# Kernel optimization log

Hardware: AMD Instinct MI355X
Metric: run time of the kernel (lower is better)

The kernel has to match this reference:

```python
import jax, jax.numpy as jnp
import numpy as np

DIM = 256
NUM_HEADS = 8
HEAD_DIM = DIM // NUM_HEADS
SCALE = HEAD_DIM ** -0.5
KSIZE = 5


def setup_inputs() -> dict:
    key = jax.random.key(0)
    ks = jax.random.split(key, 6)
    B, C, H, W = 8, DIM, 32, 32
    x = jax.random.normal(ks[0], (B, C, H, W), dtype=jnp.float32)
    qkv_w = jax.random.normal(ks[1], (3 * C, C), dtype=jnp.float32) * 0.02  # 1x1 conv, no bias
    proj_w = jax.random.normal(ks[2], (C, C), dtype=jnp.float32) * 0.02    # 1x1 conv
    proj_b = jax.random.normal(ks[3], (C,), dtype=jnp.float32) * 0.02
    lepe_w = jax.random.normal(ks[4], (C, 1, KSIZE, KSIZE), dtype=jnp.float32) * 0.02  # depthwise
    lepe_b = jax.random.normal(ks[5], (C,), dtype=jnp.float32) * 0.02
    return {"x": x, "qkv_w": qkv_w, "proj_w": proj_w, "proj_b": proj_b,
            "lepe_w": lepe_w, "lepe_b": lepe_b}


def _forward(x, qkv_w, proj_w, proj_b, lepe_w, lepe_b):
    B, C, H, W = x.shape
    N = H * W
    # 1x1 conv qkv: [B,3C,H,W]
    qkv = jnp.einsum('bchw,oc->bohw', x, qkv_w)
    q, k, v = jnp.split(qkv, 3, axis=1)
    # reshape to [B, heads, head_dim, N]
    qh = q.reshape(B, NUM_HEADS, HEAD_DIM, N)
    kh = k.reshape(B, NUM_HEADS, HEAD_DIM, N)
    vh = v.reshape(B, NUM_HEADS, HEAD_DIM, N)
    # attn = (q^T k) * scale, softmax over keys -> [B, heads, N, N]
    attn = jnp.einsum('bhdn,bhdm->bhnm', qh, kh)
    attn = jax.nn.softmax(attn * SCALE, axis=-1)
    # out = attn @ v^T -> [B, heads, N, head_dim] -> [B, C, H, W]
    out = jnp.einsum('bhnm,bhdm->bhdn', attn, vh).reshape(B, C, H, W)
    # LePE: depthwise conv on v (image layout) + residual add
    lepe = jax.lax.conv_general_dilated(
        v, lepe_w, window_strides=(1, 1),
        padding=[(KSIZE // 2, KSIZE // 2)] * 2,
        dimension_numbers=('NCHW', 'OIHW', 'NCHW'),
        feature_group_count=C) + lepe_b[None, :, None, None]
    out = out + lepe
    # 1x1 proj
    out = jnp.einsum('bchw,oc->bohw', out, proj_w) + proj_b[None, :, None, None]
    return out


def reference(x, qkv_w, proj_w, proj_b, lepe_w, lepe_b):
    return _forward(x, qkv_w, proj_w, proj_b, lepe_w, lepe_b)
```

## Files before the change

### kernel.cpp

```cpp
#include <hip/hip_runtime.h>

#define NB 8
#define NC 256
#define NN 1024

typedef unsigned short u16;
typedef unsigned int u32;
typedef __attribute__((ext_vector_type(8))) short short8;
typedef __attribute__((ext_vector_type(4))) float f32x4;

__device__ __forceinline__ u16 f2b(float f){ union{float ff;u32 i;}v; v.ff=f; u32 r=v.i+0x7FFFu+((v.i>>16)&1u); return (u16)(r>>16); }
__device__ __forceinline__ float b2f(u16 p){ union{u32 i;float f;}v; v.i=((u32)p)<<16; return v.f; }
__device__ __forceinline__ float pklo(u32 p){ union{u32 i;float f;}v; v.i=p<<16; return v.f; }
__device__ __forceinline__ float pkhi(u32 p){ union{u32 i;float f;}v; v.i=p&0xFFFF0000u; return v.f; }

#define QSC 0.25503486f

union FR { uint4 u; short8 s; };

__global__ void __launch_bounds__(256) k_cast(const float* __restrict__ x,
                                              u16* __restrict__ xt){
  const int n0 = blockIdx.x*64, c0 = blockIdx.y*128, b = blockIdx.z;
  const int tid = threadIdx.x;
  __shared__ u16 lt[64][136];
  #pragma unroll
  for (int cc = 0; cc < 4; cc++){
    const int c = c0 + cc*32 + (tid>>3);
    const int ns = (tid&7)*8;
    const float* src = x + ((size_t)(b*NC + c))*NN + n0 + ns;
    float4 a = *(const float4*)src;
    float4 d = *(const float4*)(src+4);
    const int cl = c - c0;
    lt[ns+0][cl] = f2b(a.x); lt[ns+1][cl] = f2b(a.y);
    lt[ns+2][cl] = f2b(a.z); lt[ns+3][cl] = f2b(a.w);
    lt[ns+4][cl] = f2b(d.x); lt[ns+5][cl] = f2b(d.y);
    lt[ns+6][cl] = f2b(d.z); lt[ns+7][cl] = f2b(d.w);
  }
  __syncthreads();
  #pragma unroll
  for (int p = 0; p < 4; p++){
    const int flat = p*256 + tid;
    const int row = flat >> 4, seg = flat & 15;
    uint4 d = *(uint4*)&lt[row][seg*8];
    *(uint4*)(xt + ((size_t)(b*NN + n0 + row))*NC + c0 + seg*8) = d;
  }
}

__global__ void __launch_bounds__(256) k_qkv(const float* __restrict__ wq,
                                             const u16* __restrict__ xt,
                                             u16* __restrict__ qt,
                                             u16* __restrict__ kt,
                                             u16* __restrict__ v){
  const int ot = blockIdx.x >> 6, rest = blockIdx.x & 63;
  const int nt = rest >> 3, b = rest & 7;
  const int o0 = ot*64;
  const int tid = threadIdx.x, wv = tid>>6, lane = tid&63;
  const int l15 = lane&15, quad = lane>>4;
  const int n0w = nt*128 + wv*32;
  __shared__ u16 swq[64][264];
  __shared__ u16 s2[4][32][72];
  #pragma unroll
  for (int i = 0; i < 16; i++){
    const int flat = i*256 + tid;
    const int row = flat >> 6, c4 = flat & 63;
    float4 a = *(const float4*)(wq + (size_t)(o0+row)*NC + c4*4);
    uint2 p;
    p.x = (u32)f2b(a.x) | ((u32)f2b(a.y)<<16);
    p.y = (u32)f2b(a.z) | ((u32)f2b(a.w)<<16);
    *(uint2*)&swq[row][c4*4] = p;
  }
  __syncthreads();
  f32x4 acc[4][2];
  #pragma unroll
  for (int mt = 0; mt < 4; mt++)
    #pragma unroll
    for (int n2 = 0; n2 < 2; n2++) acc[mt][n2] = (f32x4){0.f,0.f,0.f,0.f};
  const u16* xb = xt + ((size_t)(b*NN + n0w))*NC;
  for (int k0 = 0; k0 < 256; k0 += 32){
    FR af[4], bf[2];
    #pragma unroll
    for (int mt = 0; mt < 4; mt++)
      af[mt].u = *(uint4*)&swq[mt*16 + l15][k0 + quad*8];
    #pragma unroll
    for (int n2 = 0; n2 < 2; n2++)
      bf[n2].u = *(const uint4*)(xb + (size_t)(n2*16+l15)*NC + k0 + quad*8);
    #pragma unroll
    for (int mt = 0; mt < 4; mt++)
      #pragma unroll
      for (int n2 = 0; n2 < 2; n2++)
        acc[mt][n2] = __builtin_amdgcn_mfma_f32_16x16x32_bf16(af[mt].s, bf[n2].s, acc[mt][n2], 0,0,0);
  }
  if (ot < 8){
    const float sc = (ot < 4) ? QSC : 1.0f;
    u16* dstbase = (ot < 4) ? qt : kt;
    const int h0 = (ot < 4) ? (o0 >> 5) : ((o0-256) >> 5);
    #pragma unroll
    for (int mt = 0; mt < 4; mt++)
      #pragma unroll
      for (int n2 = 0; n2 < 2; n2++){
        uint2 w;
        w.x = (u32)f2b(acc[mt][n2][0]*sc) | ((u32)f2b(acc[mt][n2][1]*sc)<<16);
        w.y = (u32)f2b(acc[mt][n2][2]*sc) | ((u32)f2b(acc[mt][n2][3]*sc)<<16);
        *(uint2*)&s2[wv][n2*16+l15][mt*16+quad*4] = w;
      }
    __syncthreads();
    #pragma unroll
    for (int p = 0; p < 4; p++){
      const int u = p*64 + lane;
      const int hh = u >> 7, rem = u & 127;
      const int n_loc = rem >> 2, seg = rem & 3;
      uint4 d = *(uint4*)&s2[wv][n_loc][hh*32 + seg*8];
      u16* db = dstbase + ((size_t)(b*8 + h0 + hh)*NN + n0w + n_loc)*32 + seg*8;
      *(uint4*)db = d;
    }
  } else {
    const int c0 = o0 - 512;
    #pragma unroll
    for (int mt = 0; mt < 4; mt++)
      #pragma unroll
      for (int n2 = 0; n2 < 2; n2++)
        #pragma unroll
        for (int r = 0; r < 4; r++)
          v[(size_t)(b*NC + c0 + mt*16 + quad*4 + r)*NN + n0w + n2*16 + l15] = f2b(acc[mt][n2][r]);
  }
}

__global__ void __launch_bounds__(256, 4) k_attn(const u16* __restrict__ qt,
                                                 const u16* __restrict__ kt,
                                                 const u16* __restrict__ v,
                                                 const float* __restrict__ lw,
                                                 const float* __restrict__ lb,
                                                 u16* __restrict__ tt){
  const int qt2 = blockIdx.x >> 6, bh = blockIdx.x & 63;
  const int b = bh >> 3, h = bh & 7;
  const int tid = threadIdx.x;
  const int wv = tid >> 6, lane = tid & 63;
  const int l15 = lane & 15, quad = lane >> 4;
  const int qg = wv & 1, kh = wv >> 1;
  const int q0 = qt2*64 + qg*32;

  __shared__ u16 pb[4][2][16][40];
  __shared__ u16 vstage[6][32][38];
  __shared__ u16 s_out[2][32][36];
  __shared__ float mnum[2][32][33];
  __shared__ float mden[2][32];

  {
    const int rr = tid >> 5, lc2 = tid & 31;
    if (rr < 6){
      const int yy = qt2*2 - 2 + rr;
      u32* dst32 = (u32*)&vstage[rr][lc2][0];
      if (yy < 0 || yy > 31){
        #pragma unroll
        for (int j = 0; j < 19; j++) dst32[j] = 0;
      } else {
        const u16* src = v + ((size_t)(b*NC + h*32 + lc2))*NN + yy*32;
        uint4 a = *(const uint4*)src;
        uint4 b4 = *(const uint4*)(src+8);
        uint4 c4 = *(const uint4*)(src+16);
        uint4 d4 = *(const uint4*)(src+24);
        dst32[0] = 0;
        dst32[1]=a.x;  dst32[2]=a.y;  dst32[3]=a.z;  dst32[4]=a.w;
        dst32[5]=b4.x; dst32[6]=b4.y; dst32[7]=b4.z; dst32[8]=b4.w;
        dst32[9]=c4.x; dst32[10]=c4.y; dst32[11]=c4.z; dst32[12]=c4.w;
        dst32[13]=d4.x; dst32[14]=d4.y; dst32[15]=d4.z; dst32[16]=d4.w;
        dst32[17]=0; dst32[18]=0;
      }
    }
  }
  __syncthreads();

  const u16* qtb = qt + (size_t)bh*NN*32;
  const u16* ktb = kt + (size_t)bh*NN*32;
  const u16* vbp = v + (size_t)(b*256 + h*32)*NN;

  FR qa, qb_;
  qa.u  = *(const uint4*)(qtb + (size_t)(q0      + l15)*32 + quad*8);
  qb_.u = *(const uint4*)(qtb + (size_t)(q0 + 16 + l15)*32 + quad*8);

  f32x4 z = {0.f,0.f,0.f,0.f};
  f32x4 oA0 = z, oA1 = z, oB0 = z, oB1 = z;
  float denA[4] = {0.f,0.f,0.f,0.f}, denB[4] = {0.f,0.f,0.f,0.f};

  u16* pA = &pb[wv][0][0][0];
  u16* pB = &pb[wv][1][0][0];

  for (int it = 0; it < 16; it++){
    const int m0 = kh*512 + it*32;
    FR kf0, kf1, vf0, vf1;
    kf0.u = *(const uint4*)(ktb + (size_t)(m0      + l15)*32 + quad*8);
    kf1.u = *(const uint4*)(ktb + (size_t)(m0 + 16 + l15)*32 + quad*8);
    vf0.u = *(const uint4*)(vbp + (size_t)(l15     )*NN + m0 + quad*8);
    vf1.u = *(const uint4*)(vbp + (size_t)(16 + l15)*NN + m0 + quad*8);

    f32x4 sA0 = __builtin_amdgcn_mfma_f32_16x16x32_bf16(qa.s,  kf0.s, z, 0,0,0);
    f32x4 sA1 = __builtin_amdgcn_mfma_f32_16x16x32_bf16(qa.s,  kf1.s, z, 0,0,0);
    f32x4 sB0 = __builtin_amdgcn_mfma_f32_16x16x32_bf16(qb_.s, kf0.s, z, 0,0,0);
    f32x4 sB1 = __builtin_amdgcn_mfma_f32_16x16x32_bf16(qb_.s, kf1.s, z, 0,0,0);

    #pragma unroll
    for (int r = 0; r < 4; r++){
      float pA0 = __builtin_amdgcn_exp2f(sA0[r]);
      float pA1 = __builtin_amdgcn_exp2f(sA1[r]);
      float pB0 = __builtin_amdgcn_exp2f(sB0[r]);
      float pB1 = __builtin_amdgcn_exp2f(sB1[r]);
      denA[r] += pA0 + pA1;
      denB[r] += pB0 + pB1;
      const int row = (quad*4 + r)*40;
      pA[row + l15]      = (u16)(__float_as_uint(pA0)>>16);
      pA[row + 16 + l15] = (u16)(__float_as_uint(pA1)>>16);
      pB[row + l15]      = (u16)(__float_as_uint(pB0)>>16);
      pB[row + 16 + l15] = (u16)(__float_as_uint(pB1)>>16);
    }
    FR pfA, pfB;
    pfA.u = *(const uint4*)(pA + l15*40 + quad*8);
    pfB.u = *(const uint4*)(pB + l15*40 + quad*8);

    oA0 = __builtin_amdgcn_mfma_f32_16x16x32_bf16(pfA.s, vf0.s, oA0, 0,0,0);
    oA1 = __builtin_amdgcn_mfma_f32_16x16x32_bf16(pfA.s, vf1.s, oA1, 0,0,0);
    oB0 = __builtin_amdgcn_mfma_f32_16x16x32_bf16(pfB.s, vf0.s, oB0, 0,0,0);
    oB1 = __builtin_amdgcn_mfma_f32_16x16x32_bf16(pfB.s, vf1.s, oB1, 0,0,0);
  }
  #pragma unroll
  for (int r = 0; r < 4; r++){
    #pragma unroll
    for (int m = 1; m < 16; m <<= 1){
      denA[r] += __shfl_xor(denA[r], m);
      denB[r] += __shfl_xor(denB[r], m);
    }
  }
  __syncthreads();
  if (kh == 1){
    #pragma unroll
    for (int r = 0; r < 4; r++){
      mnum[qg][quad*4 + r][l15]          = oA0[r];
      mnum[qg][quad*4 + r][16 + l15]     = oA1[r];
      mnum[qg][16 + quad*4 + r][l15]     = oB0[r];
      mnum[qg][16 + quad*4 + r][16 + l15]= oB1[r];
    }
    if (l15 == 0){
      #pragma unroll
      for (int r = 0; r < 4; r++){
        mden[qg][quad*4 + r]      = denA[r];
        mden[qg][16 + quad*4 + r] = denB[r];
      }
    }
  }
  __syncthreads();
  if (kh == 0){
    u16* so = &s_out[qg][0][0];
    #pragma unroll
    for (int r = 0; r < 4; r++){
      const int q = quad*4 + r;
      const float dA = denA[r] + mden[qg][q];
      const float dB = denB[r] + mden[qg][16 + q];
      const float iA = 1.f/dA, iB = 1.f/dB;
      so[q*36 + l15]           = f2b((oA0[r] + mnum[qg][q][l15])*iA);
      so[q*36 + 16 + l15]      = f2b((oA1[r] + mnum[qg][q][16+l15])*iA);
      so[(q+16)*36 + l15]      = f2b((oB0[r] + mnum[qg][16+q][l15])*iB);
      so[(q+16)*36 + 16 + l15] = f2b((oB1[r] + mnum[qg][16+q][16+l15])*iB);
    }
    const int lc = lane & 31, qh = lane >> 5;
    float lep[16];
    const float lbias = lb[h*32 + lc];
    #pragma unroll
    for (int i = 0; i < 16; i++) lep[i] = lbias;
    const float* lwc = lw + (size_t)(h*32 + lc)*25;
    #pragma unroll
    for (int ky = 0; ky < 5; ky++){
      const u32* vr = (const u32*)&vstage[qg + ky][lc][0];
      float vv[20];
      #pragma unroll
      for (int jj = 0; jj < 10; jj++){
        u32 pk = vr[qh*8 + jj];
        vv[2*jj]   = pklo(pk);
        vv[2*jj+1] = pkhi(pk);
      }
      const float w0 = lwc[ky*5+0], w1 = lwc[ky*5+1], w2 = lwc[ky*5+2],
                  w3 = lwc[ky*5+3], w4 = lwc[ky*5+4];
      #pragma unroll
      for (int i = 0; i < 16; i++)
        lep[i] += w0*vv[i] + w1*vv[i+1] + w2*vv[i+2] + w3*vv[i+3] + w4*vv[i+4];
    }
    u16* tb = tt + ((size_t)(b*NN + q0))*NC + h*32;
    #pragma unroll
    for (int i = 0; i < 16; i++){
      const int q = qh*16 + i;
      tb[(size_t)q*NC + lc] = f2b(b2f(so[q*36 + lc]) + lep[i]);
    }
  }
}

__global__ void __launch_bounds__(256) k_proj(const float* __restrict__ wp,
                                              const u16* __restrict__ tt,
                                              const float* __restrict__ pbias,
                                              float* __restrict__ out){
  const int ot = blockIdx.x >> 6, rest = blockIdx.x & 63;
  const int nt = rest >> 3, b = rest & 7;
  const int o0 = ot*32;
  const int tid = threadIdx.x, wv = tid>>6, lane = tid&63;
  const int l15 = lane&15, quad = lane>>4;
  const int n0w = nt*128 + wv*32;
  __shared__ u16 swp[32][264];
  #pragma unroll
  for (int i = 0; i < 8; i++){
    const int flat = i*256 + tid;
    const int row = flat >> 6, c4 = flat & 63;
    float4 a = *(const float4*)(wp + (size_t)(o0+row)*NC + c4*4);
    uint2 p;
    p.x = (u32)f2b(a.x) | ((u32)f2b(a.y)<<16);
    p.y = (u32)f2b(a.z) | ((u32)f2b(a.w)<<16);
    *(uint2*)&swp[row][c4*4] = p;
  }
  __syncthreads();
  f32x4 acc[2][2];
  #pragma unroll
  for (int mt = 0; mt < 2; mt++)
    #pragma unroll
    for (int n2 = 0; n2 < 2; n2++) acc[mt][n2] = (f32x4){0.f,0.f,0.f,0.f};
  const u16* tb = tt + ((size_t)(b*NN + n0w))*NC;
  for (int k0 = 0; k0 < 256; k0 += 32){
    FR af[2], bf[2];
    af[0].u = *(uint4*)&swp[l15][k0 + quad*8];
    af[1].u = *(uint4*)&swp[16+l15][k0 + quad*8];
    bf[0].u = *(const uint4*)(tb + (size_t)(l15     )*NC + k0 + quad*8);
    bf[1].u = *(const uint4*)(tb + (size_t)(16 + l15)*NC + k0 + quad*8);
    #pragma unroll
    for (int mt = 0; mt < 2; mt++)
      #pragma unroll
      for (int n2 = 0; n2 < 2; n2++)
        acc[mt][n2] = __builtin_amdgcn_mfma_f32_16x16x32_bf16(af[mt].s, bf[n2].s, acc[mt][n2], 0,0,0);
  }
  float bv[2][4];
  #pragma unroll
  for (int mt = 0; mt < 2; mt++)
    #pragma unroll
    for (int r = 0; r < 4; r++) bv[mt][r] = pbias[o0 + mt*16 + quad*4 + r];
  #pragma unroll
  for (int mt = 0; mt < 2; mt++)
    #pragma unroll
    for (int n2 = 0; n2 < 2; n2++)
      #pragma unroll
      for (int r = 0; r < 4; r++)
        out[(size_t)(b*NC + o0 + mt*16 + quad*4 + r)*NN + n0w + n2*16 + l15] = acc[mt][n2][r] + bv[mt][r];
}

extern "C" void kernel_launch(void* const* d_in, const int* in_sizes, int n_in,
                              void* d_out, int out_size, void* d_ws, size_t ws_size,
                              hipStream_t stream){
  const float* x      = (const float*)d_in[0];
  const float* qkv_w  = (const float*)d_in[1];
  const float* proj_w = (const float*)d_in[2];
  const float* proj_b = (const float*)d_in[3];
  const float* lepe_w = (const float*)d_in[4];
  const float* lepe_b = (const float*)d_in[5];
  float* out = (float*)d_out;

  if (ws_size < (size_t)20*1024*1024) return;
  u16* xt = (u16*)d_ws;
  u16* qt = xt + 2097152;
  u16* kt = qt + 2097152;
  u16* v  = kt + 2097152;
  u16* tt = v  + 2097152;

  k_cast<<<dim3(16, 2, 8), 256, 0, stream>>>(x, xt);
  k_qkv <<<dim3(768),      256, 0, stream>>>(qkv_w, xt, qt, kt, v);
  k_attn<<<dim3(1024),     256, 0, stream>>>(qt, kt, v, lepe_w, lepe_b, tt);
  k_proj<<<dim3(512),      256, 0, stream>>>(proj_w, tt, proj_b, out);
}
```

Measured before the change: 123.0 us.

## Fuse four kernels into one persistent kernel with grid-wide atomic barriers

```diff
diff --git a/kernel.cpp b/kernel.cpp
--- a/kernel.cpp
+++ b/kernel.cpp
@@ -3,6 +3,7 @@
 #define NB 8
 #define NC 256
 #define NN 1024
+#define GRID_BLOCKS 768
 
 typedef unsigned short u16;
 typedef unsigned int u32;
@@ -18,331 +19,346 @@
 
 union FR { uint4 u; short8 s; };
 
-__global__ void __launch_bounds__(256) k_cast(const float* __restrict__ x,
-                                              u16* __restrict__ xt){
-  const int n0 = blockIdx.x*64, c0 = blockIdx.y*128, b = blockIdx.z;
-  const int tid = threadIdx.x;
-  __shared__ u16 lt[64][136];
-  #pragma unroll
-  for (int cc = 0; cc < 4; cc++){
-    const int c = c0 + cc*32 + (tid>>3);
-    const int ns = (tid&7)*8;
-    const float* src = x + ((size_t)(b*NC + c))*NN + n0 + ns;
-    float4 a = *(const float4*)src;
-    float4 d = *(const float4*)(src+4);
-    const int cl = c - c0;
-    lt[ns+0][cl] = f2b(a.x); lt[ns+1][cl] = f2b(a.y);
-    lt[ns+2][cl] = f2b(a.z); lt[ns+3][cl] = f2b(a.w);
-    lt[ns+4][cl] = f2b(d.x); lt[ns+5][cl] = f2b(d.y);
-    lt[ns+6][cl] = f2b(d.z); lt[ns+7][cl] = f2b(d.w);
-  }
+__device__ __forceinline__ void gbar(u32* ctr){
   __syncthreads();
-  #pragma unroll
-  for (int p = 0; p < 4; p++){
-    const int flat = p*256 + tid;
-    const int row = flat >> 4, seg = flat & 15;
-    uint4 d = *(uint4*)&lt[row][seg*8];
-    *(uint4*)(xt + ((size_t)(b*NN + n0 + row))*NC + c0 + seg*8) = d;
-  }
+  if (threadIdx.x == 0){
+    __threadfence();
+    __hip_atomic_fetch_add(ctr, 1u, __ATOMIC_ACQ_REL, __HIP_MEMORY_SCOPE_AGENT);
+    while (__hip_atomic_load(ctr, __ATOMIC_ACQUIRE, __HIP_MEMORY_SCOPE_AGENT) < (u32)GRID_BLOCKS)
+      __builtin_amdgcn_s_sleep(8);
+  }
+  __syncthreads();
 }
 
-__global__ void __launch_bounds__(256) k_qkv(const float* __restrict__ wq,
-                                             const u16* __restrict__ xt,
-                                             u16* __restrict__ qt,
-                                             u16* __restrict__ kt,
-                                             u16* __restrict__ v){
-  const int ot = blockIdx.x >> 6, rest = blockIdx.x & 63;
-  const int nt = rest >> 3, b = rest & 7;
-  const int o0 = ot*64;
-  const int tid = threadIdx.x, wv = tid>>6, lane = tid&63;
-  const int l15 = lane&15, quad = lane>>4;
-  const int n0w = nt*128 + wv*32;
-  __shared__ u16 swq[64][264];
-  __shared__ u16 s2[4][32][72];
-  #pragma unroll
-  for (int i = 0; i < 16; i++){
-    const int flat = i*256 + tid;
-    const int row = flat >> 6, c4 = flat & 63;
-    float4 a = *(const float4*)(wq + (size_t)(o0+row)*NC + c4*4);
-    uint2 p;
-    p.x = (u32)f2b(a.x) | ((u32)f2b(a.y)<<16);
-    p.y = (u32)f2b(a.z) | ((u32)f2b(a.w)<<16);
-    *(uint2*)&swq[row][c4*4] = p;
-  }
-  __syncthreads();
-  f32x4 acc[4][2];
-  #pragma unroll
-  for (int mt = 0; mt < 4; mt++)
-    #pragma unroll
-    for (int n2 = 0; n2 < 2; n2++) acc[mt][n2] = (f32x4){0.f,0.f,0.f,0.f};
-  const u16* xb = xt + ((size_t)(b*NN + n0w))*NC;
-  for (int k0 = 0; k0 < 256; k0 += 32){
-    FR af[4], bf[2];
-    #pragma unroll
-    for (int mt = 0; mt < 4; mt++)
-      af[mt].u = *(uint4*)&swq[mt*16 + l15][k0 + quad*8];
-    #pragma unroll
-    for (int n2 = 0; n2 < 2; n2++)
-      bf[n2].u = *(const uint4*)(xb + (size_t)(n2*16+l15)*NC + k0 + quad*8);
-    #pragma unroll
-    for (int mt = 0; mt < 4; mt++)
-      #pragma unroll
-      for (int n2 = 0; n2 < 2; n2++)
-        acc[mt][n2] = __builtin_amdgcn_mfma_f32_16x16x32_bf16(af[mt].s, bf[n2].s, acc[mt][n2], 0,0,0);
-  }
-  if (ot < 8){
-    const float sc = (ot < 4) ? QSC : 1.0f;
-    u16* dstbase = (ot < 4) ? qt : kt;
-    const int h0 = (ot < 4) ? (o0 >> 5) : ((o0-256) >> 5);
-    #pragma unroll
-    for (int mt = 0; mt < 4; mt++)
-      #pragma unroll
-      for (int n2 = 0; n2 < 2; n2++){
-        uint2 w;
-        w.x = (u32)f2b(acc[mt][n2][0]*sc) | ((u32)f2b(acc[mt][n2][1]*sc)<<16);
-        w.y = (u32)f2b(acc[mt][n2][2]*sc) | ((u32)f2b(acc[mt][n2][3]*sc)<<16);
-        *(uint2*)&s2[wv][n2*16+l15][mt*16+quad*4] = w;
-      }
-    __syncthreads();
-    #pragma unroll
-    for (int p = 0; p < 4; p++){
-      const int u = p*64 + lane;
-      const int hh = u >> 7, rem = u & 127;
-      const int n_loc = rem >> 2, seg = rem & 3;
-      uint4 d = *(uint4*)&s2[wv][n_loc][hh*32 + seg*8];
-      u16* db = dstbase + ((size_t)(b*8 + h0 + hh)*NN + n0w + n_loc)*32 + seg*8;
-      *(uint4*)db = d;
-    }
-  } else {
-    const int c0 = o0 - 512;
-    #pragma unroll
-    for (int mt = 0; mt < 4; mt++)
-      #pragma unroll
-      for (int n2 = 0; n2 < 2; n2++)
-        #pragma unroll
-        for (int r = 0; r < 4; r++)
-          v[(size_t)(b*NC + c0 + mt*16 + quad*4 + r)*NN + n0w + n2*16 + l15] = f2b(acc[mt][n2][r]);
-  }
-}
-
-__global__ void __launch_bounds__(256, 4) k_attn(const u16* __restrict__ qt,
-                                                 const u16* __restrict__ kt,
-                                                 const u16* __restrict__ v,
-                                                 const float* __restrict__ lw,
-                                                 const float* __restrict__ lb,
-                                                 u16* __restrict__ tt){
-  const int qt2 = blockIdx.x >> 6, bh = blockIdx.x & 63;
-  const int b = bh >> 3, h = bh & 7;
+__global__ void __launch_bounds__(256, 4) k_fused(
+    const float* __restrict__ x,
+    const float* __restrict__ wq,
+    const float* __restrict__ wp,
+    const float* __restrict__ pbias,
+    const float* __restrict__ lw,
+    const float* __restrict__ lb,
+    float* __restrict__ out,
+    u16* __restrict__ xt,
+    u16* __restrict__ qt,
+    u16* __restrict__ kt,
+    u16* __restrict__ v,
+    u16* __restrict__ tt,
+    u32* __restrict__ bar)
+{
+  __shared__ __align__(16) char smem[28160];
+  const int bx = blockIdx.x;
   const int tid = threadIdx.x;
   const int wv = tid >> 6, lane = tid & 63;
   const int l15 = lane & 15, quad = lane >> 4;
-  const int qg = wv & 1, kh = wv >> 1;
-  const int q0 = qt2*64 + qg*32;
-
-  __shared__ u16 pb[4][2][16][40];
-  __shared__ u16 vstage[6][32][38];
-  __shared__ u16 s_out[2][32][36];
-  __shared__ float mnum[2][32][33];
-  __shared__ float mden[2][32];
+
+  if (bx < 256){
+    u16* lt = (u16*)smem;
+    const int n0 = (bx & 15)*64, c0 = ((bx>>4)&1)*128, b = bx>>5;
+    #pragma unroll
+    for (int cc = 0; cc < 4; cc++){
+      const int c = c0 + cc*32 + (tid>>3);
+      const int ns = (tid&7)*8;
+      const float* src = x + ((size_t)(b*NC + c))*NN + n0 + ns;
+      float4 a = *(const float4*)src;
+      float4 d = *(const float4*)(src+4);
+      const int cl = c - c0;
+      lt[(ns+0)*136+cl] = f2b(a.x); lt[(ns+1)*136+cl] = f2b(a.y);
+      lt[(ns+2)*136+cl] = f2b(a.z); lt[(ns+3)*136+cl] = f2b(a.w);
+      lt[(ns+4)*136+cl] = f2b(d.x); lt[(ns+5)*136+cl] = f2b(d.y);
+      lt[(ns+6)*136+cl] = f2b(d.z); lt[(ns+7)*136+cl] = f2b(d.w);
+    }
+    __syncthreads();
+    #pragma unroll
+    for (int p = 0; p < 4; p++){
+      const int flat = p*256 + tid;
+      const int row = flat >> 4, seg = flat & 15;
+      uint4 d = *(uint4*)(lt + row*136 + seg*8);
+      *(uint4*)(xt + ((size_t)(b*NN + n0 + row))*NC + c0 + seg*8) = d;
+    }
+  }
+  gbar(bar + 0);
 
   {
-    const int rr = tid >> 5, lc2 = tid & 31;
-    if (rr < 6){
-      const int yy = qt2*2 - 2 + rr;
-      u32* dst32 = (u32*)&vstage[rr][lc2][0];
-      if (yy < 0 || yy > 31){
-        #pragma unroll
-        for (int j = 0; j < 19; j++) dst32[j] = 0;
-      } else {
-        const u16* src = v + ((size_t)(b*NC + h*32 + lc2))*NN + yy*32;
-        uint4 a = *(const uint4*)src;
-        uint4 b4 = *(const uint4*)(src+8);
-        uint4 c4 = *(const uint4*)(src+16);
-        uint4 d4 = *(const uint4*)(src+24);
-        dst32[0] = 0;
-        dst32[1]=a.x;  dst32[2]=a.y;  dst32[3]=a.z;  dst32[4]=a.w;
-        dst32[5]=b4.x; dst32[6]=b4.y; dst32[7]=b4.z; dst32[8]=b4.w;
-        dst32[9]=c4.x; dst32[10]=c4.y; dst32[11]=c4.z; dst32[12]=c4.w;
-        dst32[13]=d4.x; dst32[14]=d4.y; dst32[15]=d4.z; dst32[16]=d4.w;
-        dst32[17]=0; dst32[18]=0;
-      }
-    }
-  }
-  __syncthreads();
-
-  const u16* qtb = qt + (size_t)bh*NN*32;
-  const u16* ktb = kt + (size_t)bh*NN*32;
-  const u16* vbp = v + (size_t)(b*256 + h*32)*NN;
-
-  FR qa, qb_;
-  qa.u  = *(const uint4*)(qtb + (size_t)(q0      + l15)*32 + quad*8);
-  qb_.u = *(const uint4*)(qtb + (size_t)(q0 + 16 + l15)*32 + quad*8);
-
-  f32x4 z = {0.f,0.f,0.f,0.f};
-  f32x4 oA0 = z, oA1 = z, oB0 = z, oB1 = z;
-  float denA[4] = {0.f,0.f,0.f,0.f}, denB[4] = {0.f,0.f,0.f,0.f};
-
-  u16* pA = &pb[wv][0][0][0];
-  u16* pB = &pb[wv][1][0][0];
-
-  for (int it = 0; it < 16; it++){
-    const int m0 = kh*512 + it*32;
-    FR kf0, kf1, vf0, vf1;
-    kf0.u = *(const uint4*)(ktb + (size_t)(m0      + l15)*32 + quad*8);
-    kf1.u = *(const uint4*)(ktb + (size_t)(m0 + 16 + l15)*32 + quad*8);
-    vf0.u = *(const uint4*)(vbp + (size_t)(l15     )*NN + m0 + quad*8);
-    vf1.u = *(const uint4*)(vbp + (size_t)(16 + l15)*NN + m0 + quad*8);
-
-    f32x4 sA0 = __builtin_amdgcn_mfma_f32_16x16x32_bf16(qa.s,  kf0.s, z, 0,0,0);
-    f32x4 sA1 = __builtin_amdgcn_mfma_f32_16x16x32_bf16(qa.s,  kf1.s, z, 0,0,0);
-    f32x4 sB0 = __builtin_amdgcn_mfma_f32_16x16x32_bf16(qb_.s, kf0.s, z, 0,0,0);
-    f32x4 sB1 = __builtin_amdgcn_mfma_f32_16x16x32_bf16(qb_.s, kf1.s, z, 0,0,0);
-
+    const int ot = bx >> 5, nb = bx & 31;
+    const int nt = nb >> 3, b = nb & 7;
+    const int o0 = ot*32;
+    const int n0w = nt*256 + wv*64;
+    u16* swq = (u16*)smem;
+    #pragma unroll
+    for (int i = 0; i < 8; i++){
+      const int flat = i*256 + tid;
+      const int row = flat >> 6, c4 = flat & 63;
+      float4 a = *(const float4*)(wq + (size_t)(o0+row)*NC + c4*4);
+      uint2 p;
+      p.x = (u32)f2b(a.x) | ((u32)f2b(a.y)<<16);
+      p.y = (u32)f2b(a.z) | ((u32)f2b(a.w)<<16);
+      *(uint2*)(swq + row*264 + c4*4) = p;
+    }
+    __syncthreads();
+    f32x4 acc[2][4];
+    #pragma unroll
+    for (int mt = 0; mt < 2; mt++)
+      #pragma unroll
+      for (int nt2 = 0; nt2 < 4; nt2++) acc[mt][nt2] = (f32x4){0.f,0.f,0.f,0.f};
+    const u16* xb = xt + ((size_t)(b*NN + n0w))*NC;
+    for (int k0 = 0; k0 < 256; k0 += 32){
+      FR af[2], bf[4];
+      af[0].u = *(uint4*)(swq + l15*264 + k0 + quad*8);
+      af[1].u = *(uint4*)(swq + (16+l15)*264 + k0 + quad*8);
+      #pragma unroll
+      for (int nt2 = 0; nt2 < 4; nt2++)
+        bf[nt2].u = *(const uint4*)(xb + (size_t)(nt2*16+l15)*NC + k0 + quad*8);
+      #pragma unroll
+      for (int mt = 0; mt < 2; mt++)
+        #pragma unroll
+        for (int nt2 = 0; nt2 < 4; nt2++)
+          acc[mt][nt2] = __builtin_amdgcn_mfma_f32_16x16x32_bf16(af[mt].s, bf[nt2].s, acc[mt][nt2], 0,0,0);
+    }
+    __syncthreads();
+    u16* s2 = (u16*)smem;
+    if (ot < 16){
+      const float sc = (ot < 8) ? QSC : 1.0f;
+      u16* dstbase = (ot < 8) ? qt : kt;
+      const int h = (ot < 8) ? ot : ot-8;
+      #pragma unroll
+      for (int mt = 0; mt < 2; mt++)
+        #pragma unroll
+        for (int nt2 = 0; nt2 < 4; nt2++){
+          uint2 w;
+          w.x = (u32)f2b(acc[mt][nt2][0]*sc) | ((u32)f2b(acc[mt][nt2][1]*sc)<<16);
+          w.y = (u32)f2b(acc[mt][nt2][2]*sc) | ((u32)f2b(acc[mt][nt2][3]*sc)<<16);
+          *(uint2*)(s2 + ((size_t)wv*64 + nt2*16+l15)*40 + mt*16+quad*4) = w;
+        }
+      __syncthreads();
+      u16* db = dstbase + ((size_t)(b*8+h)*NN + n0w)*32;
+      #pragma unroll
+      for (int p = 0; p < 4; p++){
+        const int n_loc = p*16 + (lane>>2), seg = lane&3;
+        uint4 d = *(uint4*)(s2 + ((size_t)wv*64 + n_loc)*40 + seg*8);
+        *(uint4*)(db + (size_t)n_loc*32 + seg*8) = d;
+      }
+    } else {
+      const int c0 = o0 - 512;
+      #pragma unroll
+      for (int mt = 0; mt < 2; mt++)
+        #pragma unroll
+        for (int nt2 = 0; nt2 < 4; nt2++)
+          #pragma unroll
+          for (int r = 0; r < 4; r++)
+            v[(size_t)(b*NC + c0 + mt*16 + quad*4 + r)*NN + n0w + nt2*16 + l15] = f2b(acc[mt][nt2][r]);
+    }
+  }
+  gbar(bar + 1);
+
+  for (int task = bx; task < 1024; task += GRID_BLOCKS){
+    __syncthreads();
+    const int qt2 = task >> 6, bh = task & 63;
+    const int b = bh >> 3, h = bh & 7;
+    const int qg = wv & 1, kh = wv >> 1;
+    const int q0 = qt2*64 + qg*32;
+
+    u16* vstage = (u16*)smem;
+    u16* pbase  = (u16*)(smem + 14592);
+    float* mnum = (float*)(smem + 14592);
+    u16* s_out  = (u16*)(smem + 23040);
+    float* mden = (float*)(smem + 27648);
+
+    {
+      const int rr = tid >> 5, lc2 = tid & 31;
+      if (rr < 6){
+        const int yy = qt2*2 - 2 + rr;
+        u32* dst32 = (u32*)(vstage + ((size_t)rr*32 + lc2)*38);
+        if (yy < 0 || yy > 31){
+          #pragma unroll
+          for (int j = 0; j < 19; j++) dst32[j] = 0;
+        } else {
+          const u16* src = v + ((size_t)(b*NC + h*32 + lc2))*NN + yy*32;
+          uint4 a = *(const uint4*)src;
+          uint4 b4 = *(const uint4*)(src+8);
+          uint4 c4 = *(const uint4*)(src+16);
+          uint4 d4 = *(const uint4*)(src+24);
+          dst32[0] = 0;
+          dst32[1]=a.x;  dst32[2]=a.y;  dst32[3]=a.z;  dst32[4]=a.w;
+          dst32[5]=b4.x; dst32[6]=b4.y; dst32[7]=b4.z; dst32[8]=b4.w;
+          dst32[9]=c4.x; dst32[10]=c4.y; dst32[11]=c4.z; dst32[12]=c4.w;
+          dst32[13]=d4.x; dst32[14]=d4.y; dst32[15]=d4.z; dst32[16]=d4.w;
+          dst32[17]=0; dst32[18]=0;
+        }
+      }
+    }
+    __syncthreads();
+
+    const u16* qtb = qt + (size_t)bh*NN*32;
+    const u16* ktb = kt + (size_t)bh*NN*32;
+    const u16* vbp = v + (size_t)(b*256 + h*32)*NN;
+
+    FR qa, qb_;
+    qa.u  = *(const uint4*)(qtb + (size_t)(q0      + l15)*32 + quad*8);
+    qb_.u = *(const uint4*)(qtb + (size_t)(q0 + 16 + l15)*32 + quad*8);
+
+    f32x4 z = {0.f,0.f,0.f,0.f};
+    f32x4 oA0 = z, oA1 = z, oB0 = z, oB1 = z;
+    float denA[4] = {0.f,0.f,0.f,0.f}, denB[4] = {0.f,0.f,0.f,0.f};
+
+    u16* pA = pbase + (size_t)wv*1280;
+    u16* pB = pA + 640;
+
+    for (int it = 0; it < 16; it++){
+      const int m0 = kh*512 + it*32;
+      FR kf0, kf1, vf0, vf1;
+      kf0.u = *(const uint4*)(ktb + (size_t)(m0      + l15)*32 + quad*8);
+      kf1.u = *(const uint4*)(ktb + (size_t)(m0 + 16 + l15)*32 + quad*8);
+      vf0.u = *(const uint4*)(vbp + (size_t)(l15     )*NN + m0 + quad*8);
+      vf1.u = *(const uint4*)(vbp + (size_t)(16 + l15)*NN + m0 + quad*8);
+
+      f32x4 sA0 = __builtin_amdgcn_mfma_f32_16x16x32_bf16(qa.s,  kf0.s, z, 0,0,0);
+      f32x4 sA1 = __builtin_amdgcn_mfma_f32_16x16x32_bf16(qa.s,  kf1.s, z, 0,0,0);
+      f32x4 sB0 = __builtin_amdgcn_mfma_f32_16x16x32_bf16(qb_.s, kf0.s, z, 0,0,0);
+      f32x4 sB1 = __builtin_amdgcn_mfma_f32_16x16x32_bf16(qb_.s, kf1.s, z, 0,0,0);
+
+      #pragma unroll
+      for (int r = 0; r < 4; r++){
+        float pA0 = __builtin_amdgcn_exp2f(sA0[r]);
+        float pA1 = __builtin_amdgcn_exp2f(sA1[r]);
+        float pB0 = __builtin_amdgcn_exp2f(sB0[r]);
+        float pB1 = __builtin_amdgcn_exp2f(sB1[r]);
+        denA[r] += pA0 + pA1;
+        denB[r] += pB0 + pB1;
+        const int row = (quad*4 + r)*40;
+        pA[row + l15]      = (u16)(__float_as_uint(pA0)>>16);
+        pA[row + 16 + l15] = (u16)(__float_as_uint(pA1)>>16);
+        pB[row + l15]      = (u16)(__float_as_uint(pB0)>>16);
+        pB[row + 16 + l15] = (u16)(__float_as_uint(pB1)>>16);
+      }
+      FR pfA, pfB;
+      pfA.u = *(const uint4*)(pA + l15*40 + quad*8);
+      pfB.u = *(const uint4*)(pB + l15*40 + quad*8);
+
+      oA0 = __builtin_amdgcn_mfma_f32_16x16x32_bf16(pfA.s, vf0.s, oA0, 0,0,0);
+      oA1 = __builtin_amdgcn_mfma_f32_16x16x32_bf16(pfA.s, vf1.s, oA1, 0,0,0);
+      oB0 = __builtin_amdgcn_mfma_f32_16x16x32_bf16(pfB.s, vf0.s, oB0, 0,0,0);
+      oB1 = __builtin_amdgcn_mfma_f32_16x16x32_bf16(pfB.s, vf1.s, oB1, 0,0,0);
+    }
     #pragma unroll
     for (int r = 0; r < 4; r++){
-      float pA0 = __builtin_amdgcn_exp2f(sA0[r]);
-      float pA1 = __builtin_amdgcn_exp2f(sA1[r]);
-      float pB0 = __builtin_amdgcn_exp2f(sB0[r]);
-      float pB1 = __builtin_amdgcn_exp2f(sB1[r]);
-      denA[r] += pA0 + pA1;
-      denB[r] += pB0 + pB1;
-      const int row = (quad*4 + r)*40;
-      pA[row + l15]      = (u16)(__float_as_uint(pA0)>>16);
-      pA[row + 16 + l15] = (u16)(__float_as_uint(pA1)>>16);
-      pB[row + l15]      = (u16)(__float_as_uint(pB0)>>16);
-      pB[row + 16 + l15] = (u16)(__float_as_uint(pB1)>>16);
-    }
-    FR pfA, pfB;
-    pfA.u = *(const uint4*)(pA + l15*40 + quad*8);
-    pfB.u = *(const uint4*)(pB + l15*40 + quad*8);
-
-    oA0 = __builtin_amdgcn_mfma_f32_16x16x32_bf16(pfA.s, vf0.s, oA0, 0,0,0);
-    oA1 = __builtin_amdgcn_mfma_f32_16x16x32_bf16(pfA.s, vf1.s, oA1, 0,0,0);
-    oB0 = __builtin_amdgcn_mfma_f32_16x16x32_bf16(pfB.s, vf0.s, oB0, 0,0,0);
-    oB1 = __builtin_amdgcn_mfma_f32_16x16x32_bf16(pfB.s, vf1.s, oB1, 0,0,0);
-  }
-  #pragma unroll
-  for (int r = 0; r < 4; r++){
-    #pragma unroll
-    for (int m = 1; m < 16; m <<= 1){
-      denA[r] += __shfl_xor(denA[r], m);
-      denB[r] += __shfl_xor(denB[r], m);
-    }
-  }
-  __syncthreads();
-  if (kh == 1){
-    #pragma unroll
-    for (int r = 0; r < 4; r++){
-      mnum[qg][quad*4 + r][l15]          = oA0[r];
-      mnum[qg][quad*4 + r][16 + l15]     = oA1[r];
-      mnum[qg][16 + quad*4 + r][l15]     = oB0[r];
-      mnum[qg][16 + quad*4 + r][16 + l15]= oB1[r];
-    }
-    if (l15 == 0){
+      #pragma unroll
+      for (int m = 1; m < 16; m <<= 1){
+        denA[r] += __shfl_xor(denA[r], m);
+        denB[r] += __shfl_xor(denB[r], m);
+      }
+    }
+    __syncthreads();
+    if (kh == 1){
       #pragma unroll
       for (int r = 0; r < 4; r++){
-        mden[qg][quad*4 + r]      = denA[r];
-        mden[qg][16 + quad*4 + r] = denB[r];
-      }
-    }
-  }
-  __syncthreads();
-  if (kh == 0){
-    u16* so = &s_out[qg][0][0];
-    #pragma unroll
-    for (int r = 0; r < 4; r++){
-      const int q = quad*4 + r;
-      const float dA = denA[r] + mden[qg][q];
-      const float dB = denB[r] + mden[qg][16 + q];
-      const float iA = 1.f/dA, iB = 1.f/dB;
-      so[q*36 + l15]           = f2b((oA0[r] + mnum[qg][q][l15])*iA);
-      so[q*36 + 16 + l15]      = f2b((oA1[r] + mnum[qg][q][16+l15])*iA);
-      so[(q+16)*36 + l15]      = f2b((oB0[r] + mnum[qg][16+q][l15])*iB);
-      so[(q+16)*36 + 16 + l15] = f2b((oB1[r] + mnum[qg][16+q][16+l15])*iB);
-    }
-    const int lc = lane & 31, qh = lane >> 5;
-    float lep[16];
-    const float lbias = lb[h*32 + lc];
-    #pragma unroll
-    for (int i = 0; i < 16; i++) lep[i] = lbias;
-    const float* lwc = lw + (size_t)(h*32 + lc)*25;
-    #pragma unroll
-    for (int ky = 0; ky < 5; ky++){
-      const u32* vr = (const u32*)&vstage[qg + ky][lc][0];
-      float vv[20];
-      #pragma unroll
-      for (int jj = 0; jj < 10; jj++){
-        u32 pk = vr[qh*8 + jj];
-        vv[2*jj]   = pklo(pk);
-        vv[2*jj+1] = pkhi(pk);
-      }
-      const float w0 = lwc[ky*5+0], w1 = lwc[ky*5+1], w2 = lwc[ky*5+2],
-                  w3 = lwc[ky*5+3], w4 = lwc[ky*5+4];
-      #pragma unroll
-      for (int i = 0; i < 16; i++)
-        lep[i] += w0*vv[i] + w1*vv[i+1] + w2*vv[i+2] + w3*vv[i+3] + w4*vv[i+4];
-    }
-    u16* tb = tt + ((size_t)(b*NN + q0))*NC + h*32;
-    #pragma unroll
-    for (int i = 0; i < 16; i++){
-      const int q = qh*16 + i;
-      tb[(size_t)q*NC + lc] = f2b(b2f(so[q*36 + lc]) + lep[i]);
-    }
-  }
-}
-
-__global__ void __launch_bounds__(256) k_proj(const float* __restrict__ wp,
-                                              const u16* __restrict__ tt,
-                                              const float* __restrict__ pbias,
-                                              float* __restrict__ out){
-  const int ot = blockIdx.x >> 6, rest = blockIdx.x & 63;
-  const int nt = rest >> 3, b = rest & 7;
-  const int o0 = ot*32;
-  const int tid = threadIdx.x, wv = tid>>6, lane = tid&63;
-  const int l15 = lane&15, quad = lane>>4;
-  const int n0w = nt*128 + wv*32;
-  __shared__ u16 swp[32][264];
-  #pragma unroll
-  for (int i = 0; i < 8; i++){
-    const int flat = i*256 + tid;
-    const int row = flat >> 6, c4 = flat & 63;
-    float4 a = *(const float4*)(wp + (size_t)(o0+row)*NC + c4*4);
-    uint2 p;
-    p.x = (u32)f2b(a.x) | ((u32)f2b(a.y)<<16);
-    p.y = (u32)f2b(a.z) | ((u32)f2b(a.w)<<16);
-    *(uint2*)&swp[row][c4*4] = p;
-  }
-  __syncthreads();
-  f32x4 acc[2][2];
-  #pragma unroll
-  for (int mt = 0; mt < 2; mt++)
-    #pragma unroll
-    for (int n2 = 0; n2 < 2; n2++) acc[mt][n2] = (f32x4){0.f,0.f,0.f,0.f};
-  const u16* tb = tt + ((size_t)(b*NN + n0w))*NC;
-  for (int k0 = 0; k0 < 256; k0 += 32){
-    FR af[2], bf[2];
-    af[0].u = *(uint4*)&swp[l15][k0 + quad*8];
-    af[1].u = *(uint4*)&swp[16+l15][k0 + quad*8];
-    bf[0].u = *(const uint4*)(tb + (size_t)(l15     )*NC + k0 + quad*8);
-    bf[1].u = *(const uint4*)(tb + (size_t)(16 + l15)*NC + k0 + quad*8);
+        const int q = quad*4 + r;
+        mnum[((size_t)qg*32 + q)*33 + l15]           = oA0[r];
+        mnum[((size_t)qg*32 + q)*33 + 16 + l15]      = oA1[r];
+        mnum[((size_t)qg*32 + 16 + q)*33 + l15]      = oB0[r];
+        mnum[((size_t)qg*32 + 16 + q)*33 + 16 + l15] = oB1[r];
+      }
+      if (l15 == 0){
+        #pragma unroll
+        for (int r = 0; r < 4; r++){
+          mden[qg*32 + quad*4 + r]      = denA[r];
+          mden[qg*32 + 16 + quad*4 + r] = denB[r];
+        }
+      }
+    }
+    __syncthreads();
+    if (kh == 0){
+      u16* so = s_out + (size_t)qg*32*36;
+      #pragma unroll
+      for (int r = 0; r < 4; r++){
+        const int q = quad*4 + r;
+        const float dA = denA[r] + mden[qg*32 + q];
+        const float dB = denB[r] + mden[qg*32 + 16 + q];
+        const float iA = 1.f/dA, iB = 1.f/dB;
+        so[q*36 + l15]           = f2b((oA0[r] + mnum[((size_t)qg*32+q)*33 + l15])*iA);
+        so[q*36 + 16 + l15]      = f2b((oA1[r] + mnum[((size_t)qg*32+q)*33 + 16+l15])*iA);
+        so[(q+16)*36 + l15]      = f2b((oB0[r] + mnum[((size_t)qg*32+16+q)*33 + l15])*iB);
+        so[(q+16)*36 + 16 + l15] = f2b((oB1[r] + mnum[((size_t)qg*32+16+q)*33 + 16+l15])*iB);
+      }
+      const int lc = lane & 31, qh = lane >> 5;
+      float lep[16];
+      const float lbias = lb[h*32 + lc];
+      #pragma unroll
+      for (int i = 0; i < 16; i++) lep[i] = lbias;
+      const float* lwc = lw + (size_t)(h*32 + lc)*25;
+      #pragma unroll
+      for (int ky = 0; ky < 5; ky++){
+        const u32* vr = (const u32*)(vstage + ((size_t)(qg + ky)*32 + lc)*38);
+        float vv[20];
+        #pragma unroll
+        for (int jj = 0; jj < 10; jj++){
+          u32 pk = vr[qh*8 + jj];
+          vv[2*jj]   = pklo(pk);
+          vv[2*jj+1] = pkhi(pk);
+        }
+        const float w0 = lwc[ky*5+0], w1 = lwc[ky*5+1], w2 = lwc[ky*5+2],
+                    w3 = lwc[ky*5+3], w4 = lwc[ky*5+4];
+        #pragma unroll
+        for (int i = 0; i < 16; i++)
+          lep[i] += w0*vv[i] + w1*vv[i+1] + w2*vv[i+2] + w3*vv[i+3] + w4*vv[i+4];
+      }
+      u16* tb = tt + ((size_t)(b*NN + q0))*NC + h*32;
+      #pragma unroll
+      for (int i = 0; i < 16; i++){
+        const int q = qh*16 + i;
+        tb[(size_t)q*NC + lc] = f2b(b2f(so[q*36 + lc]) + lep[i]);
+      }
+    }
+  }
+  gbar(bar + 2);
+
+  if (bx < 512){
+    const int ot = bx >> 6, rest = bx & 63;
+    const int nt = rest >> 3, b = rest & 7;
+    const int o0 = ot*32;
+    const int n0w = nt*128 + wv*32;
+    u16* swp = (u16*)smem;
+    #pragma unroll
+    for (int i = 0; i < 8; i++){
+      const int flat = i*256 + tid;
+      const int row = flat >> 6, c4 = flat & 63;
+      float4 a = *(const float4*)(wp + (size_t)(o0+row)*NC + c4*4);
+      uint2 p;
+      p.x = (u32)f2b(a.x) | ((u32)f2b(a.y)<<16);
+      p.y = (u32)f2b(a.z) | ((u32)f2b(a.w)<<16);
+      *(uint2*)(swp + row*264 + c4*4) = p;
+    }
+    __syncthreads();
+    f32x4 acc[2][2];
     #pragma unroll
     for (int mt = 0; mt < 2; mt++)
       #pragma unroll
+      for (int n2 = 0; n2 < 2; n2++) acc[mt][n2] = (f32x4){0.f,0.f,0.f,0.f};
+    const u16* tb = tt + ((size_t)(b*NN + n0w))*NC;
+    for (int k0 = 0; k0 < 256; k0 += 32){
+      FR af[2], bf[2];
+      af[0].u = *(uint4*)(swp + l15*264 + k0 + quad*8);
+      af[1].u = *(uint4*)(swp + (16+l15)*264 + k0 + quad*8);
+      bf[0].u = *(const uint4*)(tb + (size_t)(l15     )*NC + k0 + quad*8);
+      bf[1].u = *(const uint4*)(tb + (size_t)(16 + l15)*NC + k0 + quad*8);
+      #pragma unroll
+      for (int mt = 0; mt < 2; mt++)
+        #pragma unroll
+        for (int n2 = 0; n2 < 2; n2++)
+          acc[mt][n2] = __builtin_amdgcn_mfma_f32_16x16x32_bf16(af[mt].s, bf[n2].s, acc[mt][n2], 0,0,0);
+    }
+    float bv[2][4];
+    #pragma unroll
+    for (int mt = 0; mt < 2; mt++)
+      #pragma unroll
+      for (int r = 0; r < 4; r++) bv[mt][r] = pbias[o0 + mt*16 + quad*4 + r];
+    #pragma unroll
+    for (int mt = 0; mt < 2; mt++)
+      #pragma unroll
       for (int n2 = 0; n2 < 2; n2++)
-        acc[mt][n2] = __builtin_amdgcn_mfma_f32_16x16x32_bf16(af[mt].s, bf[n2].s, acc[mt][n2], 0,0,0);
-  }
-  float bv[2][4];
-  #pragma unroll
-  for (int mt = 0; mt < 2; mt++)
-    #pragma unroll
-    for (int r = 0; r < 4; r++) bv[mt][r] = pbias[o0 + mt*16 + quad*4 + r];
-  #pragma unroll
-  for (int mt = 0; mt < 2; mt++)
-    #pragma unroll
-    for (int n2 = 0; n2 < 2; n2++)
-      #pragma unroll
-      for (int r = 0; r < 4; r++)
-        out[(size_t)(b*NC + o0 + mt*16 + quad*4 + r)*NN + n0w + n2*16 + l15] = acc[mt][n2][r] + bv[mt][r];
+        #pragma unroll
+        for (int r = 0; r < 4; r++)
+          out[(size_t)(b*NC + o0 + mt*16 + quad*4 + r)*NN + n0w + n2*16 + l15] = acc[mt][n2][r] + bv[mt][r];
+  }
 }
 
 extern "C" void kernel_launch(void* const* d_in, const int* in_sizes, int n_in,
@@ -356,15 +372,16 @@
   const float* lepe_b = (const float*)d_in[5];
   float* out = (float*)d_out;
 
-  if (ws_size < (size_t)20*1024*1024) return;
+  if (ws_size < (size_t)20*1024*1024 + 256) return;
   u16* xt = (u16*)d_ws;
   u16* qt = xt + 2097152;
   u16* kt = qt + 2097152;
   u16* v  = kt + 2097152;
   u16* tt = v  + 2097152;
-
-  k_cast<<<dim3(16, 2, 8), 256, 0, stream>>>(x, xt);
-  k_qkv <<<dim3(768),      256, 0, stream>>>(qkv_w, xt, qt, kt, v);
-  k_attn<<<dim3(1024),     256, 0, stream>>>(qt, kt, v, lepe_w, lepe_b, tt);
-  k_proj<<<dim3(512),      256, 0, stream>>>(proj_w, tt, proj_b, out);
+  u32* bar = (u32*)(tt + 2097152);
+
+  hipMemsetAsync(bar, 0, 256, stream);
+  k_fused<<<dim3(GRID_BLOCKS), 256, 0, stream>>>(x, qkv_w, proj_w, proj_b,
+                                                 lepe_w, lepe_b, out,
+                                                 xt, qt, kt, v, tt, bar);
 }
```

After: 487.9 us. +296.6%, slower.
